# Performance work log

Measured on AMD Instinct MI355X. Metric: run time of the kernel, lower is better.

The kernel has to match this reference:

```python
import jax, jax.numpy as jnp
import numpy as np
from math import sqrt

I = 1024  # input_size
H = 1024  # hidden_size
B = 4096  # batch


def setup_inputs() -> dict:
    key = jax.random.key(0)
    ks = jax.random.split(key, 12)
    a = 1.0 / sqrt(H)
    u = lambda k, shape: jax.random.uniform(k, shape, jnp.float32, -a, a)
    return {
        "x": jax.random.normal(ks[0], (B, I), jnp.float32),
        "hx": jax.random.normal(ks[1], (B, H), jnp.float32),
        "cx": jax.random.normal(ks[2], (B, H), jnp.float32),
        "weight_ih": u(ks[3], (4 * H, I)),
        "weight_hh": u(ks[4], (4 * H, H)),
        "bias_ih": u(ks[5], (4 * H,)),
        "bias_hh": u(ks[6], (4 * H,)),
        "W_peephole_i": u(ks[7], (H, H)),
        "W_peephole_f": u(ks[8], (H, H)),
        "W_peephole_o": u(ks[9], (H, H)),
    }


def reference(x, hx, cx, weight_ih, weight_hh, bias_ih, bias_hh,
              W_peephole_i, W_peephole_f, W_peephole_o):
    # gates: [B, 4H]
    gates = x @ weight_ih.T + bias_ih + hx @ weight_hh.T + bias_hh
    ingate, forgetgate, cellgate, outgate = jnp.split(gates, 4, axis=1)
    # F.linear(cx, W * eye) == cx * diag(W)  (diagonal peephole)
    ingate = jax.nn.sigmoid(ingate + cx * jnp.diagonal(W_peephole_i))
    forgetgate = jax.nn.sigmoid(forgetgate + cx * jnp.diagonal(W_peephole_f))
    cellgate = jnp.tanh(cellgate)
    cy = forgetgate * cx + ingate * cellgate
    # NOTE: original code reuses W_peephole_f for the output gate (faithful to source)
    outgate = jax.nn.sigmoid(outgate + cy * jnp.diagonal(W_peephole_f))
    hy = outgate * jnp.tanh(cy)
    return (hy, cy)
```

## Files before the change

kernel.cpp:

```cpp
#include <hip/hip_runtime.h>
#include <hip/hip_bf16.h>
#include <cstdint>


namespace {

constexpr int H   = 1024;
constexpr int K2  = 2048;
constexpr int BSZ = 4096;
constexpr size_t OUT_CY = (size_t)BSZ * H;

typedef __attribute__((ext_vector_type(8))) short bf16x8;
typedef __attribute__((ext_vector_type(4))) float f32x4;

__device__ __forceinline__ unsigned short f2bf(float f) {
  union { float f; uint32_t u; } v; v.f = f;
  uint32_t u = v.u;
  u += 0x7FFFu + ((u >> 16) & 1u);
  return (unsigned short)(u >> 16);
}

__device__ __forceinline__ float sigm(float x) {
  return 1.0f / (1.0f + __expf(-x));
}
__device__ __forceinline__ float tanh_fast(float x) {
  return 1.0f - 2.0f / (1.0f + __expf(2.0f * x));
}

__device__ __forceinline__ void gload_lds16(const void* g, void* l) {
  __builtin_amdgcn_global_load_lds(
      (const __attribute__((address_space(1))) void*)g,
      (__attribute__((address_space(3))) void*)l, 16, 0, 0);
}

}

__global__ __launch_bounds__(256) void cast_kernel(
    const float* __restrict__ x, const float* __restrict__ hx,
    const float* __restrict__ wih, const float* __restrict__ whh,
    unsigned short* __restrict__ A, unsigned short* __restrict__ W) {
  int b = blockIdx.x;
  bool isW = b >= 8192;
  int t = (isW ? b - 8192 : b) * 256 + threadIdx.x;
  int idx = t * 4;
  int n = idx >> 11;
  int k = idx & 2047;
  const float* s0 = isW ? wih : x;
  const float* s1 = isW ? whh : hx;
  const float* src = (k < H) ? (s0 + (size_t)n * H + k)
                             : (s1 + (size_t)n * H + (k - H));
  float4 v = *(const float4*)src;
  ushort4 o;
  o.x = f2bf(v.x); o.y = f2bf(v.y); o.z = f2bf(v.z); o.w = f2bf(v.w);
  if (isW) {
    int g = n >> 10, h = n & 1023;
    int np = ((h >> 5) << 7) + (g << 5) + (h & 31);
    *(ushort4*)(W + (size_t)np * K2 + k) = o;
  } else {
    *(ushort4*)(A + idx) = o;
  }
}

__global__ __launch_bounds__(128, 2) void lstm_fused_gemm(
    const unsigned short* __restrict__ A,
    const unsigned short* __restrict__ W,
    const float* __restrict__ cx,
    const float* __restrict__ bias_ih, const float* __restrict__ bias_hh,
    const float* __restrict__ Wpi, const float* __restrict__ Wpf,
    float* __restrict__ out) {
  __shared__ __align__(16) unsigned short As[128 * 64];
  __shared__ __align__(16) unsigned short Ws[128 * 64];

  const int tid  = threadIdx.x;
  const int lane = tid & 63;
  const int wave = tid >> 6;
  const int m0 = blockIdx.x * 128;
  const int h0 = blockIdx.y * 32;
  const int w0 = blockIdx.y * 128;

  const int srow = tid >> 3;
  const int scol = (((tid & 7) ^ (srow & 7)) << 3);

  f32x4 acc[4][8];
#pragma unroll
  for (int i = 0; i < 4; ++i)
#pragma unroll
    for (int j = 0; j < 8; ++j)
      acc[i][j] = (f32x4){0.f, 0.f, 0.f, 0.f};

  const int col  = lane & 15;
  const int quad = lane >> 4;
  const int kq   = quad * 8;

  for (int kt = 0; kt < K2 / 64; ++kt) {
    const int kb = kt * 64;
    __syncthreads();
#pragma unroll
    for (int p = 0; p < 8; ++p) {
      const int row = p * 16 + srow;
      const int ldsoff = p * 1024 + wave * 512;
      gload_lds16(A + (size_t)(m0 + row) * K2 + kb + scol, &As[ldsoff]);
      gload_lds16(W + (size_t)(w0 + row) * K2 + kb + scol, &Ws[ldsoff]);
    }
    __syncthreads();

#pragma unroll
    for (int ks = 0; ks < 2; ++ks) {
      const int kk = ks * 32 + kq;
      bf16x8 a[4], b[8];
#pragma unroll
      for (int i = 0; i < 4; ++i) {
        const int R = wave * 64 + i * 16 + col;
        a[i] = *(const bf16x8*)&As[R * 64 + (((kk >> 3) ^ (R & 7)) << 3)];
      }
#pragma unroll
      for (int j = 0; j < 8; ++j) {
        const int R = j * 16 + col;
        b[j] = *(const bf16x8*)&Ws[R * 64 + (((kk >> 3) ^ (R & 7)) << 3)];
      }
#pragma unroll
      for (int i = 0; i < 4; ++i)
#pragma unroll
        for (int j = 0; j < 8; ++j)
          acc[i][j] = __builtin_amdgcn_mfma_f32_16x16x32_bf16(a[i], b[j], acc[i][j], 0, 0, 0);
    }
  }

#pragma unroll
  for (int hh = 0; hh < 2; ++hh) {
    const int h = h0 + hh * 16 + col;
    const float bi = bias_ih[h]         + bias_hh[h];
    const float bf = bias_ih[H + h]     + bias_hh[H + h];
    const float bc = bias_ih[2 * H + h] + bias_hh[2 * H + h];
    const float bo = bias_ih[3 * H + h] + bias_hh[3 * H + h];
    const float di = Wpi[(size_t)h * (H + 1)];
    const float df = Wpf[(size_t)h * (H + 1)];
#pragma unroll
    for (int i = 0; i < 4; ++i) {
#pragma unroll
      for (int r = 0; r < 4; ++r) {
        const int m = m0 + wave * 64 + i * 16 + quad * 4 + r;
        const float c  = cx[(size_t)m * H + h];
        const float ip = acc[i][0 + hh][r] + bi;
        const float fp = acc[i][2 + hh][r] + bf;
        const float cp = acc[i][4 + hh][r] + bc;
        const float op = acc[i][6 + hh][r] + bo;
        const float ig = sigm(ip + c * di);
        const float fg = sigm(fp + c * df);
        const float cg = tanh_fast(cp);
        const float cy = fg * c + ig * cg;
        const float og = sigm(op + cy * df);
        const float hy = og * tanh_fast(cy);
        out[(size_t)m * H + h] = hy;
        out[OUT_CY + (size_t)m * H + h] = cy;
      }
    }
  }
}

extern "C" void kernel_launch(void* const* d_in, const int* in_sizes, int n_in,
                              void* d_out, int out_size, void* d_ws, size_t ws_size,
                              hipStream_t stream) {
  const float* x   = (const float*)d_in[0];
  const float* hx  = (const float*)d_in[1];
  const float* cx  = (const float*)d_in[2];
  const float* wih = (const float*)d_in[3];
  const float* whh = (const float*)d_in[4];
  const float* bih = (const float*)d_in[5];
  const float* bhh = (const float*)d_in[6];
  const float* wpi = (const float*)d_in[7];
  const float* wpf = (const float*)d_in[8];
  float* out = (float*)d_out;

  unsigned short* Abf = (unsigned short*)d_ws;
  unsigned short* Wbf = Abf + (size_t)BSZ * K2;

  cast_kernel<<<16384, 256, 0, stream>>>(x, hx, wih, whh, Abf, Wbf);

  dim3 grid(BSZ / 128, H / 32);
  lstm_fused_gemm<<<grid, 128, 0, stream>>>(Abf, Wbf, cx, bih, bhh, wpi, wpf, out);
}
```

Baseline: 220.8 us.

## Use 256x256 tiles with 8 waves and double-buffered LDS prefetch pipeline

The fused GEMM moves from 128x128 tiles with 2 waves to 256x256 tiles with 8 waves. It double-buffers the bf16 tiles in LDS, issuing global-to-LDS loads two K-steps ahead and interleaving them with MFMA phases under explicit waitcnt, barriers and setprio. The weight interleave changes to 16-row gate groups so each wave owns all four gates for 16 hidden units, and the cast kernel converts 8 elements per thread. The aim is more data reuse and hiding load latency behind compute. The cost is 128KB of LDS per block and much heavier hand scheduling, which can hurt occupancy or correctness.

```diff
diff --git a/kernel.cpp b/kernel.cpp
--- a/kernel.cpp
+++ b/kernel.cpp
@@ -1,5 +1,4 @@
 #include <hip/hip_runtime.h>
-#include <hip/hip_bf16.h>
 #include <cstdint>
 
 
@@ -12,6 +11,7 @@
 
 typedef __attribute__((ext_vector_type(8))) short bf16x8;
 typedef __attribute__((ext_vector_type(4))) float f32x4;
+typedef __attribute__((ext_vector_type(8))) unsigned short u16x8;
 
 __device__ __forceinline__ unsigned short f2bf(float f) {
   union { float f; uint32_t u; } v; v.f = f;
@@ -40,120 +40,164 @@
     const float* __restrict__ wih, const float* __restrict__ whh,
     unsigned short* __restrict__ A, unsigned short* __restrict__ W) {
   int b = blockIdx.x;
-  bool isW = b >= 8192;
-  int t = (isW ? b - 8192 : b) * 256 + threadIdx.x;
-  int idx = t * 4;
+  bool isW = b >= 4096;
+  int t = (isW ? b - 4096 : b) * 256 + threadIdx.x;
+  int idx = t * 8;
   int n = idx >> 11;
   int k = idx & 2047;
   const float* s0 = isW ? wih : x;
   const float* s1 = isW ? whh : hx;
   const float* src = (k < H) ? (s0 + (size_t)n * H + k)
                              : (s1 + (size_t)n * H + (k - H));
-  float4 v = *(const float4*)src;
-  ushort4 o;
-  o.x = f2bf(v.x); o.y = f2bf(v.y); o.z = f2bf(v.z); o.w = f2bf(v.w);
+  float4 v0 = *(const float4*)src;
+  float4 v1 = *(const float4*)(src + 4);
+  u16x8 o;
+  o[0] = f2bf(v0.x); o[1] = f2bf(v0.y); o[2] = f2bf(v0.z); o[3] = f2bf(v0.w);
+  o[4] = f2bf(v1.x); o[5] = f2bf(v1.y); o[6] = f2bf(v1.z); o[7] = f2bf(v1.w);
   if (isW) {
-    int g = n >> 10, h = n & 1023;
-    int np = ((h >> 5) << 7) + (g << 5) + (h & 31);
-    *(ushort4*)(W + (size_t)np * K2 + k) = o;
+    int g = n >> 10, hh = n & 1023;
+    int np = ((hh >> 4) << 6) + (g << 4) + (hh & 15);
+    *(u16x8*)(W + (size_t)np * K2 + k) = o;
   } else {
-    *(ushort4*)(A + idx) = o;
+    *(u16x8*)(A + (size_t)idx) = o;
   }
 }
 
-__global__ __launch_bounds__(128, 2) void lstm_fused_gemm(
+__global__ __launch_bounds__(512, 2) void lstm_fused_gemm(
     const unsigned short* __restrict__ A,
     const unsigned short* __restrict__ W,
     const float* __restrict__ cx,
     const float* __restrict__ bias_ih, const float* __restrict__ bias_hh,
     const float* __restrict__ Wpi, const float* __restrict__ Wpf,
     float* __restrict__ out) {
-  __shared__ __align__(16) unsigned short As[128 * 64];
-  __shared__ __align__(16) unsigned short Ws[128 * 64];
+  __shared__ __align__(16) unsigned short lds[2 * 32768];
 
   const int tid  = threadIdx.x;
   const int lane = tid & 63;
   const int wave = tid >> 6;
-  const int m0 = blockIdx.x * 128;
-  const int h0 = blockIdx.y * 32;
-  const int w0 = blockIdx.y * 128;
-
-  const int srow = tid >> 3;
-  const int scol = (((tid & 7) ^ (srow & 7)) << 3);
-
-  f32x4 acc[4][8];
-#pragma unroll
-  for (int i = 0; i < 4; ++i)
-#pragma unroll
-    for (int j = 0; j < 8; ++j)
-      acc[i][j] = (f32x4){0.f, 0.f, 0.f, 0.f};
+  const int wm   = wave >> 2;
+  const int wn   = wave & 3;
+  const int m0 = blockIdx.x * 256;
+  const int w0 = blockIdx.y * 256;
+
+  const int srow   = tid >> 3;
+  const int schunk = ((tid & 7) ^ (srow & 7)) << 3;
 
   const int col  = lane & 15;
   const int quad = lane >> 4;
-  const int kq   = quad * 8;
-
-  for (int kt = 0; kt < K2 / 64; ++kt) {
-    const int kb = kt * 64;
-    __syncthreads();
-#pragma unroll
-    for (int p = 0; p < 8; ++p) {
-      const int row = p * 16 + srow;
-      const int ldsoff = p * 1024 + wave * 512;
-      gload_lds16(A + (size_t)(m0 + row) * K2 + kb + scol, &As[ldsoff]);
-      gload_lds16(W + (size_t)(w0 + row) * K2 + kb + scol, &Ws[ldsoff]);
+
+  const unsigned short* Asrc = A + (size_t)(m0 + srow) * K2 + schunk;
+  const unsigned short* Wsrc = W + (size_t)(w0 + srow) * K2 + schunk;
+  const int ldsdst = wave * 512;
+
+  f32x4 acc[8][4];
+#pragma unroll
+  for (int i = 0; i < 8; ++i)
+#pragma unroll
+    for (int j = 0; j < 4; ++j)
+      acc[i][j] = (f32x4){0.f, 0.f, 0.f, 0.f};
+
+  auto stA = [&](int kt, int buf, int p) {
+    gload_lds16(Asrc + (size_t)p * 64 * K2 + kt * 64,
+                &lds[buf * 32768 + p * 4096 + ldsdst]);
+  };
+  auto stB = [&](int kt, int buf, int p) {
+    gload_lds16(Wsrc + (size_t)p * 64 * K2 + kt * 64,
+                &lds[buf * 32768 + 16384 + p * 4096 + ldsdst]);
+  };
+
+#pragma unroll
+  for (int p = 0; p < 4; ++p) stA(0, 0, p);
+#pragma unroll
+  for (int p = 0; p < 4; ++p) stB(0, 0, p);
+#pragma unroll
+  for (int p = 0; p < 4; ++p) stA(1, 1, p);
+#pragma unroll
+  for (int p = 0; p < 4; ++p) stB(1, 1, p);
+  asm volatile("s_waitcnt vmcnt(8)" ::: "memory");
+  __builtin_amdgcn_sched_barrier(0);
+  __builtin_amdgcn_s_barrier();
+
+  const int aoff = (wm * 128 + col) * 64;
+  const int boff = 16384 + (wn * 64 + col) * 64;
+  const int kch0 = ((quad ^ (col & 7)) << 3);
+  const int kch1 = (((4 + quad) ^ (col & 7)) << 3);
+
+  for (int kt = 0; kt < 32; ++kt) {
+    const int buf = kt & 1;
+    const unsigned short* Lb = &lds[buf * 32768];
+    const bool pf = (kt + 2 < 32);
+    bf16x8 bfr[4][2];
+#pragma unroll
+    for (int q = 0; q < 4; ++q) {
+      bf16x8 afr[2][2];
+      if (q == 0) {
+#pragma unroll
+        for (int j = 0; j < 4; ++j) {
+          bfr[j][0] = *(const bf16x8*)&Lb[boff + j * 1024 + kch0];
+          bfr[j][1] = *(const bf16x8*)&Lb[boff + j * 1024 + kch1];
+        }
+      }
+#pragma unroll
+      for (int i2 = 0; i2 < 2; ++i2) {
+        afr[i2][0] = *(const bf16x8*)&Lb[aoff + (2 * q + i2) * 1024 + kch0];
+        afr[i2][1] = *(const bf16x8*)&Lb[aoff + (2 * q + i2) * 1024 + kch1];
+      }
+      if (q == 1 && pf) { stB(kt + 2, buf, 0); stB(kt + 2, buf, 1); }
+      if (q == 2 && pf) { stB(kt + 2, buf, 2); stB(kt + 2, buf, 3); }
+      if (q == 3 && pf) { stA(kt + 2, buf, 0); stA(kt + 2, buf, 2); }
+      __builtin_amdgcn_s_barrier();
+      asm volatile("s_waitcnt lgkmcnt(0)" ::: "memory");
+      __builtin_amdgcn_sched_barrier(0);
+      __builtin_amdgcn_s_setprio(1);
+#pragma unroll
+      for (int i2 = 0; i2 < 2; ++i2)
+#pragma unroll
+        for (int j = 0; j < 4; ++j) {
+          acc[2 * q + i2][j] = __builtin_amdgcn_mfma_f32_16x16x32_bf16(
+              afr[i2][0], bfr[j][0], acc[2 * q + i2][j], 0, 0, 0);
+          acc[2 * q + i2][j] = __builtin_amdgcn_mfma_f32_16x16x32_bf16(
+              afr[i2][1], bfr[j][1], acc[2 * q + i2][j], 0, 0, 0);
+        }
+      __builtin_amdgcn_s_setprio(0);
+      __builtin_amdgcn_s_barrier();
     }
-    __syncthreads();
-
-#pragma unroll
-    for (int ks = 0; ks < 2; ++ks) {
-      const int kk = ks * 32 + kq;
-      bf16x8 a[4], b[8];
-#pragma unroll
-      for (int i = 0; i < 4; ++i) {
-        const int R = wave * 64 + i * 16 + col;
-        a[i] = *(const bf16x8*)&As[R * 64 + (((kk >> 3) ^ (R & 7)) << 3)];
-      }
-#pragma unroll
-      for (int j = 0; j < 8; ++j) {
-        const int R = j * 16 + col;
-        b[j] = *(const bf16x8*)&Ws[R * 64 + (((kk >> 3) ^ (R & 7)) << 3)];
-      }
-#pragma unroll
-      for (int i = 0; i < 4; ++i)
-#pragma unroll
-        for (int j = 0; j < 8; ++j)
-          acc[i][j] = __builtin_amdgcn_mfma_f32_16x16x32_bf16(a[i], b[j], acc[i][j], 0, 0, 0);
+    if (pf) {
+      stA(kt + 2, buf, 1); stA(kt + 2, buf, 3);
+      asm volatile("s_waitcnt vmcnt(8)" ::: "memory");
+    } else {
+      asm volatile("s_waitcnt vmcnt(0)" ::: "memory");
     }
+    __builtin_amdgcn_sched_barrier(0);
+    __builtin_amdgcn_s_barrier();
   }
 
-#pragma unroll
-  for (int hh = 0; hh < 2; ++hh) {
-    const int h = h0 + hh * 16 + col;
-    const float bi = bias_ih[h]         + bias_hh[h];
-    const float bf = bias_ih[H + h]     + bias_hh[H + h];
-    const float bc = bias_ih[2 * H + h] + bias_hh[2 * H + h];
-    const float bo = bias_ih[3 * H + h] + bias_hh[3 * H + h];
-    const float di = Wpi[(size_t)h * (H + 1)];
-    const float df = Wpf[(size_t)h * (H + 1)];
-#pragma unroll
-    for (int i = 0; i < 4; ++i) {
-#pragma unroll
-      for (int r = 0; r < 4; ++r) {
-        const int m = m0 + wave * 64 + i * 16 + quad * 4 + r;
-        const float c  = cx[(size_t)m * H + h];
-        const float ip = acc[i][0 + hh][r] + bi;
-        const float fp = acc[i][2 + hh][r] + bf;
-        const float cp = acc[i][4 + hh][r] + bc;
-        const float op = acc[i][6 + hh][r] + bo;
-        const float ig = sigm(ip + c * di);
-        const float fg = sigm(fp + c * df);
-        const float cg = tanh_fast(cp);
-        const float cy = fg * c + ig * cg;
-        const float og = sigm(op + cy * df);
-        const float hy = og * tanh_fast(cy);
-        out[(size_t)m * H + h] = hy;
-        out[OUT_CY + (size_t)m * H + h] = cy;
-      }
+  const int h = blockIdx.y * 64 + wn * 16 + col;
+  const float bi  = bias_ih[h]         + bias_hh[h];
+  const float bf_ = bias_ih[H + h]     + bias_hh[H + h];
+  const float bc  = bias_ih[2 * H + h] + bias_hh[2 * H + h];
+  const float bo  = bias_ih[3 * H + h] + bias_hh[3 * H + h];
+  const float di = Wpi[(size_t)h * (H + 1)];
+  const float df = Wpf[(size_t)h * (H + 1)];
+  const int mbase = m0 + wm * 128 + quad * 4;
+#pragma unroll
+  for (int i = 0; i < 8; ++i) {
+#pragma unroll
+    for (int r = 0; r < 4; ++r) {
+      const int m = mbase + i * 16 + r;
+      const float c  = cx[(size_t)m * H + h];
+      const float ip = acc[i][0][r] + bi;
+      const float fp = acc[i][1][r] + bf_;
+      const float cp = acc[i][2][r] + bc;
+      const float op = acc[i][3][r] + bo;
+      const float ig = sigm(ip + c * di);
+      const float fg = sigm(fp + c * df);
+      const float cg = tanh_fast(cp);
+      const float cy = fg * c + ig * cg;
+      const float og = sigm(op + cy * df);
+      const float hy = og * tanh_fast(cy);
+      out[(size_t)m * H + h] = hy;
+      out[OUT_CY + (size_t)m * H + h] = cy;
     }
   }
 }
@@ -175,8 +219,8 @@
   unsigned short* Abf = (unsigned short*)d_ws;
   unsigned short* Wbf = Abf + (size_t)BSZ * K2;
 
-  cast_kernel<<<16384, 256, 0, stream>>>(x, hx, wih, whh, Abf, Wbf);
-
-  dim3 grid(BSZ / 128, H / 32);
-  lstm_fused_gemm<<<grid, 128, 0, stream>>>(Abf, Wbf, cx, bih, bhh, wpi, wpf, out);
-}
+  cast_kernel<<<8192, 256, 0, stream>>>(x, hx, wih, whh, Abf, Wbf);
+
+  dim3 grid(BSZ / 256, (4 * H) / 256);
+  lstm_fused_gemm<<<grid, 512, 0, stream>>>(Abf, Wbf, cx, bih, bhh, wpi, wpf, out);
+}
```

Result: faster. 206.7 us (-6.4%).
